# Kernel optimization log

Hardware: AMD Instinct MI355X
Metric: run time of the kernel (lower is better)

Reference implementation:

```python
import jax, jax.numpy as jnp
import numpy as np

B, T, D = 4096, 64, 256       # expressions, max tokens per expression, encoding dim
N_SYM, N_OCC = 20000, 131072  # symbols, symbol occurrences


def setup_inputs() -> dict:
    key = jax.random.key(0)
    k1, k2, k3, k4, k5 = jax.random.split(key, 5)
    # unique flattened occurrence positions -> deterministic scatter
    rng = np.random.default_rng(0)
    flat_pos = rng.permutation(B * T)[:N_OCC].astype(np.int64)
    return {
        "expressions_encodings": jax.random.normal(k1, (B, T, D), dtype=jnp.float32),
        "symbols_encodings": jax.random.normal(k2, (N_SYM, D), dtype=jnp.float32),
        "Wf": jax.random.normal(k3, (D, 2 * D), dtype=jnp.float32) * 0.05,
        "bf": jnp.zeros((D,), dtype=jnp.float32),
        "Wa": jax.random.normal(k4, (D, 2 * D), dtype=jnp.float32) * 0.05,
        "ba": jnp.zeros((D,), dtype=jnp.float32),
        "expr_idx": jnp.asarray(flat_pos // T),
        "token_idx": jnp.asarray(flat_pos % T),
        "symbol_idx": jax.random.randint(k5, (N_OCC,), 0, N_SYM, dtype=jnp.int64),
    }


def reference(expressions_encodings, symbols_encodings, Wf, bf, Wa, ba,
              expr_idx, token_idx, symbol_idx):
    b, t, d = expressions_encodings.shape
    flat = expressions_encodings.reshape(b * t, d)            # [B*T, D]
    occ_pos = t * expr_idx + token_idx                        # [N_OCC]
    prev = flat[occ_pos]                                      # gather: [N_OCC, D]
    upd = symbols_encodings[symbol_idx]                       # gather: [N_OCC, D]
    concat = jnp.concatenate([prev, upd], axis=-1)            # [N_OCC, 2D]
    forget = jax.nn.sigmoid(concat @ Wf.T + bf)               # forget gate
    add = jax.nn.sigmoid(concat @ Wa.T + ba)                  # add gate
    new_occ = forget * prev + add * upd                       # gated update
    out = flat.at[occ_pos].set(new_occ)                       # scatter back
    return out.reshape(b, t, d)
```

## Files before the change

kernel.cpp:

```cpp
#include <hip/hip_runtime.h>

typedef __attribute__((ext_vector_type(8))) short short8;
typedef __attribute__((ext_vector_type(4))) short short4v;
typedef __attribute__((ext_vector_type(4))) float floatx4;

__device__ __forceinline__ unsigned short f2bf(float f) {
    unsigned int u = __float_as_uint(f);
    u += 0x7FFFu + ((u >> 16) & 1u);
    return (unsigned short)(u >> 16);
}
__device__ __forceinline__ float bf2f(unsigned short s) {
    return __uint_as_float(((unsigned int)s) << 16);
}
__device__ __forceinline__ float sigmoidf(float x) {
    return 1.f / (1.f + __expf(-x));
}

__global__ __launch_bounds__(256)
void convert_w_kernel(const float* __restrict__ Wf,
                      const float* __restrict__ Wa,
                      short* __restrict__ wswz)
{
    int id = blockIdx.x * 256 + threadIdx.x;
    int slot = id & 63;
    int ks   = (id >> 6) & 15;
    int g    = id >> 10;
    int l15  = slot & 15, lk = slot >> 4;
    const float* base = (g < 16) ? (Wf + (long)(g * 16 + l15) * 512)
                                 : (Wa + (long)((g - 16) * 16 + l15) * 512);
    const float* src = base + ks * 32 + lk * 8;
    floatx4 w0 = *(const floatx4*)src;
    floatx4 w1 = *(const floatx4*)(src + 4);
    short8 o;
    o[0] = (short)f2bf(w0[0]); o[1] = (short)f2bf(w0[1]);
    o[2] = (short)f2bf(w0[2]); o[3] = (short)f2bf(w0[3]);
    o[4] = (short)f2bf(w1[0]); o[5] = (short)f2bf(w1[1]);
    o[6] = (short)f2bf(w1[2]); o[7] = (short)f2bf(w1[3]);
    *(short8*)(wswz + (long)id * 8) = o;
}

__global__ __launch_bounds__(256)
void mark_kernel(const int* __restrict__ ei, const int* __restrict__ ti,
                 unsigned char* __restrict__ flags, int n)
{
    int i = blockIdx.x * 256 + threadIdx.x;
    if (i < n) flags[64 * ei[i] + ti[i]] = 1;
}

__global__ __launch_bounds__(256)
void copy_rest_kernel(const float* __restrict__ flat,
                      const unsigned char* __restrict__ flags,
                      float* __restrict__ out, int nrows)
{
    const int lane = threadIdx.x & 63;
    const int w0   = (blockIdx.x * 256 + threadIdx.x) >> 6;
    const int nw   = (gridDim.x * 256) >> 6;
    for (int row = w0; row < nrows; row += nw) {
        if (flags[row]) continue;
        const floatx4* s = (const floatx4*)(flat + (long)row * 256);
        floatx4*       o = (floatx4*)(out + (long)row * 256);
        o[lane] = s[lane];
    }
}

__global__ __launch_bounds__(512, 4)
void gate_gemm_kernel(const float* __restrict__ flat,
                      const float* __restrict__ syms,
                      const float* __restrict__ bfb,
                      const float* __restrict__ bab,
                      const int* __restrict__ expr_idx,
                      const int* __restrict__ token_idx,
                      const int* __restrict__ sym_idx,
                      const short* __restrict__ wswz,
                      float* __restrict__ out)
{
    __shared__ __align__(16) short A_lds[64][520];
    __shared__ int rowbuf[64];
    __shared__ int symbuf[64];

    const int tid  = threadIdx.x;
    const int occ0 = blockIdx.x * 64;

    if (tid < 64) {
        int occ = occ0 + tid;
        rowbuf[tid] = 64 * expr_idx[occ] + token_idx[occ];
        symbuf[tid] = sym_idx[occ];
    }
    __syncthreads();

    {
        const int srow = tid >> 3;
        const int se   = tid & 7;
        const float* prow = flat + (long)rowbuf[srow] * 256;
        const float* urow = syms + (long)symbuf[srow] * 256;
        #pragma unroll
        for (int it = 0; it < 8; ++it) {
            const int k = (se + it * 8) * 4;
            floatx4 v = *(const floatx4*)(prow + k);
            short4v sv;
            sv[0] = (short)f2bf(v[0]); sv[1] = (short)f2bf(v[1]);
            sv[2] = (short)f2bf(v[2]); sv[3] = (short)f2bf(v[3]);
            *(short4v*)&A_lds[srow][k] = sv;
        }
        #pragma unroll
        for (int it = 0; it < 8; ++it) {
            const int k = (se + it * 8) * 4;
            floatx4 v = *(const floatx4*)(urow + k);
            short4v sv;
            sv[0] = (short)f2bf(v[0]); sv[1] = (short)f2bf(v[1]);
            sv[2] = (short)f2bf(v[2]); sv[3] = (short)f2bf(v[3]);
            *(short4v*)&A_lds[srow][256 + k] = sv;
        }
    }
    __syncthreads();

    const int lane = tid & 63;
    const int wv   = tid >> 6;
    const int l15  = lane & 15;
    const int lk   = lane >> 4;

    floatx4 acc[4][4];
    #pragma unroll
    for (int mi = 0; mi < 4; ++mi)
        #pragma unroll
        for (int c = 0; c < 4; ++c)
            acc[mi][c] = (floatx4){0.f, 0.f, 0.f, 0.f};

    const short8* wsv = (const short8*)wswz;

    #pragma unroll
    for (int ks = 0; ks < 16; ++ks) {
        short8 cb[4];
        #pragma unroll
        for (int mi = 0; mi < 4; ++mi)
            cb[mi] = *(const short8*)&A_lds[mi * 16 + l15][ks * 32 + lk * 8];

        #pragma unroll
        for (int c = 0; c < 4; ++c) {
            const int g = (c < 2) ? (wv * 2 + c) : (16 + wv * 2 + (c - 2));
            short8 wf = wsv[(g * 16 + ks) * 64 + lane];
            #pragma unroll
            for (int mi = 0; mi < 4; ++mi)
                acc[mi][c] = __builtin_amdgcn_mfma_f32_16x16x32_bf16(
                    wf, cb[mi], acc[mi][c], 0, 0, 0);
        }
    }

    #pragma unroll
    for (int c = 0; c < 2; ++c) {
        const int d0 = wv * 32 + c * 16 + lk * 4;
        const floatx4 bfv = *(const floatx4*)(bfb + d0);
        const floatx4 bav = *(const floatx4*)(bab + d0);
        #pragma unroll
        for (int mi = 0; mi < 4; ++mi) {
            const int m = mi * 16 + l15;
            short4v pv = *(const short4v*)&A_lds[m][d0];
            short4v uv = *(const short4v*)&A_lds[m][256 + d0];
            floatx4 res;
            #pragma unroll
            for (int j = 0; j < 4; ++j) {
                float fg = sigmoidf(acc[mi][c][j]     + bfv[j]);
                float ag = sigmoidf(acc[mi][c + 2][j] + bav[j]);
                res[j] = fg * bf2f((unsigned short)pv[j])
                       + ag * bf2f((unsigned short)uv[j]);
            }
            *(floatx4*)(out + (long)rowbuf[m] * 256 + d0) = res;
        }
    }
}

extern "C" void kernel_launch(void* const* d_in, const int* in_sizes, int n_in,
                              void* d_out, int out_size, void* d_ws, size_t ws_size,
                              hipStream_t stream) {
    const float* flat = (const float*)d_in[0];
    const float* syms = (const float*)d_in[1];
    const float* Wf   = (const float*)d_in[2];
    const float* bf   = (const float*)d_in[3];
    const float* Wa   = (const float*)d_in[4];
    const float* ba   = (const float*)d_in[5];
    const int* ei     = (const int*)d_in[6];
    const int* ti     = (const int*)d_in[7];
    const int* si     = (const int*)d_in[8];
    float* out        = (float*)d_out;

    short* wswz          = (short*)d_ws;
    unsigned char* flags = (unsigned char*)d_ws + 512 * 1024;

    const int n_occ = in_sizes[6];
    const int nrows = out_size / 256;

    hipMemsetAsync(flags, 0, nrows, stream);
    mark_kernel<<<(n_occ + 255) / 256, 256, 0, stream>>>(ei, ti, flags, n_occ);

    convert_w_kernel<<<128, 256, 0, stream>>>(Wf, Wa, wswz);

    gate_gemm_kernel<<<n_occ / 64, 512, 0, stream>>>(flat, syms, bf, ba,
                                                     ei, ti, si, wswz, out);

    copy_rest_kernel<<<2048, 256, 0, stream>>>(flat, flags, out, nrows);
}
```

Before: 241.5 us.

## Split gather into separate bf16 staging kernel and async-load it into GEMM

Splits the fused gate GEMM in two. A new gather kernel collects the prev and symbol rows, converts them to bf16, and writes a dense swizzled A matrix to workspace. The GEMM kernel then fills LDS with direct global-to-LDS async loads using an XOR swizzle to avoid bank conflicts. The aim is to take the irregular gather and conversion off the MFMA kernel's critical path, at the cost of an extra 128 MB-scale round trip through workspace plus one more launch. The old fused path stays as a fallback when the workspace is too small.

```diff
diff --git a/kernel.cpp b/kernel.cpp
--- a/kernel.cpp
+++ b/kernel.cpp
@@ -1,4 +1,5 @@
 #include <hip/hip_runtime.h>
+#include <stdint.h>
 
 typedef __attribute__((ext_vector_type(8))) short short8;
 typedef __attribute__((ext_vector_type(4))) short short4v;
@@ -14,6 +15,13 @@
 }
 __device__ __forceinline__ float sigmoidf(float x) {
     return 1.f / (1.f + __expf(-x));
+}
+
+__device__ __forceinline__ void async_load16(const short* g, short* l) {
+    __builtin_amdgcn_global_load_lds(
+        (const __attribute__((address_space(1))) unsigned int*)(uintptr_t)g,
+        (__attribute__((address_space(3))) unsigned int*)(uintptr_t)l,
+        16, 0, 0);
 }
 
 __global__ __launch_bounds__(256)
@@ -63,16 +71,132 @@
     }
 }
 
+__global__ __launch_bounds__(256)
+void gather_convert_kernel(const float* __restrict__ flat,
+                           const float* __restrict__ syms,
+                           const int* __restrict__ ei,
+                           const int* __restrict__ ti,
+                           const int* __restrict__ si,
+                           short* __restrict__ Adense, int n_occ)
+{
+    const int lane = threadIdx.x & 63;
+    const int wid  = (blockIdx.x * 256 + threadIdx.x) >> 6;
+    const int nw   = (gridDim.x * 256) >> 6;
+    for (int occ = wid; occ < n_occ; occ += nw) {
+        const int row = 64 * ei[occ] + ti[occ];
+        const int sym = si[occ];
+        const float* src = (lane < 32)
+            ? (flat + (long)row * 256 + lane * 8)
+            : (syms + (long)sym * 256 + (lane - 32) * 8);
+        floatx4 v0 = *(const floatx4*)src;
+        floatx4 v1 = *(const floatx4*)(src + 4);
+        short8 o;
+        o[0] = (short)f2bf(v0[0]); o[1] = (short)f2bf(v0[1]);
+        o[2] = (short)f2bf(v0[2]); o[3] = (short)f2bf(v0[3]);
+        o[4] = (short)f2bf(v1[0]); o[5] = (short)f2bf(v1[1]);
+        o[6] = (short)f2bf(v1[2]); o[7] = (short)f2bf(v1[3]);
+        const int co = lane ^ (occ & 7);
+        *(short8*)(Adense + (long)occ * 512 + co * 8) = o;
+    }
+}
+
 __global__ __launch_bounds__(512, 4)
-void gate_gemm_kernel(const float* __restrict__ flat,
-                      const float* __restrict__ syms,
+void gemm_gate_kernel(const short* __restrict__ Adense,
                       const float* __restrict__ bfb,
                       const float* __restrict__ bab,
                       const int* __restrict__ expr_idx,
                       const int* __restrict__ token_idx,
-                      const int* __restrict__ sym_idx,
                       const short* __restrict__ wswz,
                       float* __restrict__ out)
+{
+    __shared__ __align__(16) short A_lds[64 * 512];
+
+    const int tid  = threadIdx.x;
+    const int occ0 = blockIdx.x * 64;
+
+    {
+        const short* gbase = Adense + (long)occ0 * 512;
+        const int wub = (tid & ~63) * 8;
+        #pragma unroll
+        for (int i = 0; i < 8; ++i)
+            async_load16(gbase + i * 4096 + tid * 8, A_lds + i * 4096 + wub);
+    }
+    asm volatile("s_waitcnt vmcnt(0)" ::: "memory");
+    __syncthreads();
+
+    const int lane = tid & 63;
+    const int wv   = tid >> 6;
+    const int l15  = lane & 15;
+    const int lk   = lane >> 4;
+
+    floatx4 acc[4][4];
+    #pragma unroll
+    for (int mi = 0; mi < 4; ++mi)
+        #pragma unroll
+        for (int c = 0; c < 4; ++c)
+            acc[mi][c] = (floatx4){0.f, 0.f, 0.f, 0.f};
+
+    const short8* wsv = (const short8*)wswz;
+
+    #pragma unroll
+    for (int ks = 0; ks < 16; ++ks) {
+        short8 cb[4];
+        #pragma unroll
+        for (int mi = 0; mi < 4; ++mi) {
+            const int m = mi * 16 + l15;
+            const int ch = ((ks << 2) | lk) ^ (m & 7);
+            cb[mi] = *(const short8*)&A_lds[m * 512 + (ch << 3)];
+        }
+        #pragma unroll
+        for (int c = 0; c < 4; ++c) {
+            const int g = (c < 2) ? (wv * 2 + c) : (16 + wv * 2 + (c - 2));
+            short8 wf = wsv[(g * 16 + ks) * 64 + lane];
+            #pragma unroll
+            for (int mi = 0; mi < 4; ++mi)
+                acc[mi][c] = __builtin_amdgcn_mfma_f32_16x16x32_bf16(
+                    wf, cb[mi], acc[mi][c], 0, 0, 0);
+        }
+    }
+
+    #pragma unroll
+    for (int c = 0; c < 2; ++c) {
+        const int d0 = wv * 32 + c * 16 + lk * 4;
+        const floatx4 bfv = *(const floatx4*)(bfb + d0);
+        const floatx4 bav = *(const floatx4*)(bab + d0);
+        const int cp = d0 >> 3;
+        const int cu = 32 + (d0 >> 3);
+        const int sub = (lk & 1) * 4;
+        #pragma unroll
+        for (int mi = 0; mi < 4; ++mi) {
+            const int m = mi * 16 + l15;
+            const int sw = m & 7;
+            short4v pv = *(const short4v*)&A_lds[m * 512 + ((cp ^ sw) << 3) + sub];
+            short4v uv = *(const short4v*)&A_lds[m * 512 + ((cu ^ sw) << 3) + sub];
+            floatx4 res;
+            #pragma unroll
+            for (int j = 0; j < 4; ++j) {
+                float fg = sigmoidf(acc[mi][c][j]     + bfv[j]);
+                float ag = sigmoidf(acc[mi][c + 2][j] + bav[j]);
+                res[j] = fg * bf2f((unsigned short)pv[j])
+                       + ag * bf2f((unsigned short)uv[j]);
+            }
+            const int occ = occ0 + m;
+            const long row = 64 * expr_idx[occ] + token_idx[occ];
+            *(floatx4*)(out + row * 256 + d0) = res;
+        }
+    }
+}
+
+__global__ __launch_bounds__(512, 4)
+void gate_gemm_fused_kernel(const float* __restrict__ flat,
+                            const float* __restrict__ syms,
+                            const float* __restrict__ bfb,
+                            const float* __restrict__ bab,
+                            const int* __restrict__ expr_idx,
+                            const int* __restrict__ token_idx,
+                            const int* __restrict__ sym_idx,
+                            const short* __restrict__ wswz,
+                            float* __restrict__ out)
 {
     __shared__ __align__(16) short A_lds[64][520];
     __shared__ int rowbuf[64];
@@ -87,7 +211,6 @@
         symbuf[tid] = sym_idx[occ];
     }
     __syncthreads();
-
     {
         const int srow = tid >> 3;
         const int se   = tid & 7;
@@ -134,7 +257,6 @@
         #pragma unroll
         for (int mi = 0; mi < 4; ++mi)
             cb[mi] = *(const short8*)&A_lds[mi * 16 + l15][ks * 32 + lk * 8];
-
         #pragma unroll
         for (int c = 0; c < 4; ++c) {
             const int g = (c < 2) ? (wv * 2 + c) : (16 + wv * 2 + (c - 2));
@@ -145,7 +267,6 @@
                     wf, cb[mi], acc[mi][c], 0, 0, 0);
         }
     }
-
     #pragma unroll
     for (int c = 0; c < 2; ++c) {
         const int d0 = wv * 32 + c * 16 + lk * 4;
@@ -185,17 +306,25 @@
 
     short* wswz          = (short*)d_ws;
     unsigned char* flags = (unsigned char*)d_ws + 512 * 1024;
+    short* Adense        = (short*)((char*)d_ws + (1 << 20));
 
     const int n_occ = in_sizes[6];
     const int nrows = out_size / 256;
 
     hipMemsetAsync(flags, 0, nrows, stream);
     mark_kernel<<<(n_occ + 255) / 256, 256, 0, stream>>>(ei, ti, flags, n_occ);
-
     convert_w_kernel<<<128, 256, 0, stream>>>(Wf, Wa, wswz);
 
-    gate_gemm_kernel<<<n_occ / 64, 512, 0, stream>>>(flat, syms, bf, ba,
-                                                     ei, ti, si, wswz, out);
+    const size_t need = (size_t)(1 << 20) + (size_t)n_occ * 1024;
+    if (ws_size >= need) {
+        gather_convert_kernel<<<4096, 256, 0, stream>>>(flat, syms, ei, ti, si,
+                                                        Adense, n_occ);
+        gemm_gate_kernel<<<n_occ / 64, 512, 0, stream>>>(Adense, bf, ba,
+                                                         ei, ti, wswz, out);
+    } else {
+        gate_gemm_fused_kernel<<<n_occ / 64, 512, 0, stream>>>(
+            flat, syms, bf, ba, ei, ti, si, wswz, out);
+    }
 
     copy_rest_kernel<<<2048, 256, 0, stream>>>(flat, flags, out, nrows);
 }
```

Result: slower. 281.5 us (+16.6%).

## Make gate GEMM persistent with register-prefetched gather pipeline and swizzled LDS

Applied to the files above, without the earlier changes.

Replaces the one-tile-per-block gate GEMM with a persistent kernel of 256 blocks of 1024 threads. Each block walks several 64-occurrence tiles and prefetches the next tile's gathered rows into registers while the MFMAs for the current tile run. The A tile in LDS loses its padding and uses an XOR swizzle to avoid bank conflicts, and each wave now owns 16 output columns instead of 32. The memset is replaced with a small zeroing kernel. The trade-offs are fewer resident blocks, higher register pressure, and indices being re-read from global memory in the epilogue.

```diff
diff --git a/kernel.cpp b/kernel.cpp
--- a/kernel.cpp
+++ b/kernel.cpp
@@ -40,6 +40,12 @@
 }
 
 __global__ __launch_bounds__(256)
+void zero_flags_kernel(unsigned int* __restrict__ flags)
+{
+    flags[blockIdx.x * 256 + threadIdx.x] = 0u;
+}
+
+__global__ __launch_bounds__(256)
 void mark_kernel(const int* __restrict__ ei, const int* __restrict__ ti,
                  unsigned char* __restrict__ flags, int n)
 {
@@ -63,108 +69,131 @@
     }
 }
 
-__global__ __launch_bounds__(512, 4)
-void gate_gemm_kernel(const float* __restrict__ flat,
+__global__ __launch_bounds__(1024, 4)
+void gate_pipe_kernel(const float* __restrict__ flat,
                       const float* __restrict__ syms,
                       const float* __restrict__ bfb,
                       const float* __restrict__ bab,
-                      const int* __restrict__ expr_idx,
-                      const int* __restrict__ token_idx,
-                      const int* __restrict__ sym_idx,
+                      const int* __restrict__ ei,
+                      const int* __restrict__ ti,
+                      const int* __restrict__ si,
                       const short* __restrict__ wswz,
-                      float* __restrict__ out)
-{
-    __shared__ __align__(16) short A_lds[64][520];
-    __shared__ int rowbuf[64];
-    __shared__ int symbuf[64];
+                      float* __restrict__ out,
+                      int ntiles, int tpb)
+{
+    __shared__ __align__(16) short A_lds[64 * 512];
 
     const int tid  = threadIdx.x;
-    const int occ0 = blockIdx.x * 64;
-
-    if (tid < 64) {
-        int occ = occ0 + tid;
-        rowbuf[tid] = 64 * expr_idx[occ] + token_idx[occ];
-        symbuf[tid] = sym_idx[occ];
-    }
-    __syncthreads();
-
-    {
-        const int srow = tid >> 3;
-        const int se   = tid & 7;
-        const float* prow = flat + (long)rowbuf[srow] * 256;
-        const float* urow = syms + (long)symbuf[srow] * 256;
-        #pragma unroll
-        for (int it = 0; it < 8; ++it) {
-            const int k = (se + it * 8) * 4;
-            floatx4 v = *(const floatx4*)(prow + k);
-            short4v sv;
-            sv[0] = (short)f2bf(v[0]); sv[1] = (short)f2bf(v[1]);
-            sv[2] = (short)f2bf(v[2]); sv[3] = (short)f2bf(v[3]);
-            *(short4v*)&A_lds[srow][k] = sv;
-        }
-        #pragma unroll
-        for (int it = 0; it < 8; ++it) {
-            const int k = (se + it * 8) * 4;
-            floatx4 v = *(const floatx4*)(urow + k);
-            short4v sv;
-            sv[0] = (short)f2bf(v[0]); sv[1] = (short)f2bf(v[1]);
-            sv[2] = (short)f2bf(v[2]); sv[3] = (short)f2bf(v[3]);
-            *(short4v*)&A_lds[srow][256 + k] = sv;
-        }
-    }
-    __syncthreads();
+    const int srow = tid >> 4;
+    const int se   = tid & 15;
+    const int sw   = srow & 7;
 
     const int lane = tid & 63;
-    const int wv   = tid >> 6;
+    const int w    = tid >> 6;
     const int l15  = lane & 15;
     const int lk   = lane >> 4;
 
-    floatx4 acc[4][4];
-    #pragma unroll
-    for (int mi = 0; mi < 4; ++mi)
-        #pragma unroll
-        for (int c = 0; c < 4; ++c)
-            acc[mi][c] = (floatx4){0.f, 0.f, 0.f, 0.f};
-
+    const int tfirst = blockIdx.x * tpb;
+
+    floatx4 v[8];
+    auto issue = [&](int tile) {
+        const int occ = tile * 64 + srow;
+        const long row = 64 * ei[occ] + ti[occ];
+        const long sym = si[occ];
+        const float* pr = flat + row * 256;
+        const float* ur = syms + sym * 256;
+        v[0] = *(const floatx4*)(pr + se * 8);
+        v[1] = *(const floatx4*)(pr + se * 8 + 4);
+        v[2] = *(const floatx4*)(pr + (se + 16) * 8);
+        v[3] = *(const floatx4*)(pr + (se + 16) * 8 + 4);
+        v[4] = *(const floatx4*)(ur + se * 8);
+        v[5] = *(const floatx4*)(ur + se * 8 + 4);
+        v[6] = *(const floatx4*)(ur + (se + 16) * 8);
+        v[7] = *(const floatx4*)(ur + (se + 16) * 8 + 4);
+    };
+
+    if (tfirst < ntiles) issue(tfirst);
+
+    const int d0 = w * 16 + lk * 4;
+    const floatx4 bfv = *(const floatx4*)(bfb + d0);
+    const floatx4 bav = *(const floatx4*)(bab + d0);
     const short8* wsv = (const short8*)wswz;
 
-    #pragma unroll
-    for (int ks = 0; ks < 16; ++ks) {
-        short8 cb[4];
-        #pragma unroll
-        for (int mi = 0; mi < 4; ++mi)
-            cb[mi] = *(const short8*)&A_lds[mi * 16 + l15][ks * 32 + lk * 8];
-
-        #pragma unroll
-        for (int c = 0; c < 4; ++c) {
-            const int g = (c < 2) ? (wv * 2 + c) : (16 + wv * 2 + (c - 2));
-            short8 wf = wsv[(g * 16 + ks) * 64 + lane];
+    for (int t = 0; t < tpb; ++t) {
+        const int tile = tfirst + t;
+        if (tile >= ntiles) break;
+
+        short8 s8[4];
+        #pragma unroll
+        for (int h = 0; h < 4; ++h) {
+            floatx4 a = v[h * 2], b = v[h * 2 + 1];
+            short8 o;
+            o[0] = (short)f2bf(a[0]); o[1] = (short)f2bf(a[1]);
+            o[2] = (short)f2bf(a[2]); o[3] = (short)f2bf(a[3]);
+            o[4] = (short)f2bf(b[0]); o[5] = (short)f2bf(b[1]);
+            o[6] = (short)f2bf(b[2]); o[7] = (short)f2bf(b[3]);
+            s8[h] = o;
+        }
+
+        __syncthreads();
+
+        #pragma unroll
+        for (int h = 0; h < 4; ++h) {
+            const int chunk = (se + ((h & 1) << 4) + ((h >> 1) << 5)) ^ sw;
+            *(short8*)&A_lds[srow * 512 + chunk * 8] = s8[h];
+        }
+
+        __syncthreads();
+
+        if (t + 1 < tpb && tile + 1 < ntiles) issue(tile + 1);
+
+        floatx4 acc[4][2];
+        #pragma unroll
+        for (int mi = 0; mi < 4; ++mi) {
+            acc[mi][0] = (floatx4){0.f, 0.f, 0.f, 0.f};
+            acc[mi][1] = (floatx4){0.f, 0.f, 0.f, 0.f};
+        }
+
+        #pragma unroll
+        for (int ks = 0; ks < 16; ++ks) {
+            short8 cb[4];
+            #pragma unroll
+            for (int mi = 0; mi < 4; ++mi) {
+                const int m  = mi * 16 + l15;
+                const int ch = (ks * 4 + lk) ^ (m & 7);
+                cb[mi] = *(const short8*)&A_lds[m * 512 + ch * 8];
+            }
+            const short8 wff = wsv[(w * 16 + ks) * 64 + lane];
             #pragma unroll
             for (int mi = 0; mi < 4; ++mi)
-                acc[mi][c] = __builtin_amdgcn_mfma_f32_16x16x32_bf16(
-                    wf, cb[mi], acc[mi][c], 0, 0, 0);
-        }
-    }
-
-    #pragma unroll
-    for (int c = 0; c < 2; ++c) {
-        const int d0 = wv * 32 + c * 16 + lk * 4;
-        const floatx4 bfv = *(const floatx4*)(bfb + d0);
-        const floatx4 bav = *(const floatx4*)(bab + d0);
+                acc[mi][0] = __builtin_amdgcn_mfma_f32_16x16x32_bf16(
+                    wff, cb[mi], acc[mi][0], 0, 0, 0);
+            const short8 wfa = wsv[((16 + w) * 16 + ks) * 64 + lane];
+            #pragma unroll
+            for (int mi = 0; mi < 4; ++mi)
+                acc[mi][1] = __builtin_amdgcn_mfma_f32_16x16x32_bf16(
+                    wfa, cb[mi], acc[mi][1], 0, 0, 0);
+        }
+
         #pragma unroll
         for (int mi = 0; mi < 4; ++mi) {
-            const int m = mi * 16 + l15;
-            short4v pv = *(const short4v*)&A_lds[m][d0];
-            short4v uv = *(const short4v*)&A_lds[m][256 + d0];
+            const int m   = mi * 16 + l15;
+            const int occ = tile * 64 + m;
+            const long row = 64 * ei[occ] + ti[occ];
+            const int cp = (d0 >> 3) ^ (m & 7);
+            const int cu = (32 + (d0 >> 3)) ^ (m & 7);
+            const int sub = d0 & 7;
+            short4v pv = *(const short4v*)&A_lds[m * 512 + cp * 8 + sub];
+            short4v uv = *(const short4v*)&A_lds[m * 512 + cu * 8 + sub];
             floatx4 res;
             #pragma unroll
             for (int j = 0; j < 4; ++j) {
-                float fg = sigmoidf(acc[mi][c][j]     + bfv[j]);
-                float ag = sigmoidf(acc[mi][c + 2][j] + bav[j]);
+                float fg = sigmoidf(acc[mi][0][j] + bfv[j]);
+                float ag = sigmoidf(acc[mi][1][j] + bav[j]);
                 res[j] = fg * bf2f((unsigned short)pv[j])
                        + ag * bf2f((unsigned short)uv[j]);
             }
-            *(floatx4*)(out + (long)rowbuf[m] * 256 + d0) = res;
+            *(floatx4*)(out + row * 256 + d0) = res;
         }
     }
 }
@@ -189,13 +218,16 @@
     const int n_occ = in_sizes[6];
     const int nrows = out_size / 256;
 
-    hipMemsetAsync(flags, 0, nrows, stream);
+    zero_flags_kernel<<<nrows / 1024, 256, 0, stream>>>((unsigned int*)flags);
     mark_kernel<<<(n_occ + 255) / 256, 256, 0, stream>>>(ei, ti, flags, n_occ);
-
     convert_w_kernel<<<128, 256, 0, stream>>>(Wf, Wa, wswz);
 
-    gate_gemm_kernel<<<n_occ / 64, 512, 0, stream>>>(flat, syms, bf, ba,
-                                                     ei, ti, si, wswz, out);
+    const int ntiles = n_occ / 64;
+    const int nblk   = 256;
+    const int tpb    = (ntiles + nblk - 1) / nblk;
+    gate_pipe_kernel<<<nblk, 1024, 0, stream>>>(flat, syms, bf, ba,
+                                                ei, ti, si, wswz, out,
+                                                ntiles, tpb);
 
     copy_rest_kernel<<<2048, 256, 0, stream>>>(flat, flags, out, nrows);
 }
```

Result: slower. 304.5 us (+26.1%).

## Fuse copy-rest into gate GEMM kernel with interleaved blocks and swizzled LDS

Applied to the files above, without the earlier changes.

Merges the untouched-row copy kernel into the gate GEMM launch, interleaving copy blocks among GEMM tiles so the copy traffic overlaps with compute and one launch is saved. The A tile is stored densely in LDS with an XOR swizzle in place of padding. Weight fragments are prefetched one k-step ahead, and the M dimension is processed in two halves to cut accumulator registers. The memset is replaced by a small zeroing kernel. Costs are extra index reloads in the epilogue and a more complex block-role mapping.

```diff
diff --git a/kernel.cpp b/kernel.cpp
--- a/kernel.cpp
+++ b/kernel.cpp
@@ -40,6 +40,12 @@
 }
 
 __global__ __launch_bounds__(256)
+void zero_flags_kernel(unsigned int* __restrict__ flags)
+{
+    flags[blockIdx.x * 256 + threadIdx.x] = 0u;
+}
+
+__global__ __launch_bounds__(256)
 void mark_kernel(const int* __restrict__ ei, const int* __restrict__ ti,
                  unsigned char* __restrict__ flags, int n)
 {
@@ -47,124 +53,155 @@
     if (i < n) flags[64 * ei[i] + ti[i]] = 1;
 }
 
-__global__ __launch_bounds__(256)
-void copy_rest_kernel(const float* __restrict__ flat,
-                      const unsigned char* __restrict__ flags,
-                      float* __restrict__ out, int nrows)
-{
-    const int lane = threadIdx.x & 63;
-    const int w0   = (blockIdx.x * 256 + threadIdx.x) >> 6;
-    const int nw   = (gridDim.x * 256) >> 6;
-    for (int row = w0; row < nrows; row += nw) {
-        if (flags[row]) continue;
-        const floatx4* s = (const floatx4*)(flat + (long)row * 256);
-        floatx4*       o = (floatx4*)(out + (long)row * 256);
-        o[lane] = s[lane];
-    }
-}
-
 __global__ __launch_bounds__(512, 4)
-void gate_gemm_kernel(const float* __restrict__ flat,
-                      const float* __restrict__ syms,
-                      const float* __restrict__ bfb,
-                      const float* __restrict__ bab,
-                      const int* __restrict__ expr_idx,
-                      const int* __restrict__ token_idx,
-                      const int* __restrict__ sym_idx,
-                      const short* __restrict__ wswz,
-                      float* __restrict__ out)
-{
-    __shared__ __align__(16) short A_lds[64][520];
-    __shared__ int rowbuf[64];
-    __shared__ int symbuf[64];
-
-    const int tid  = threadIdx.x;
-    const int occ0 = blockIdx.x * 64;
-
-    if (tid < 64) {
-        int occ = occ0 + tid;
-        rowbuf[tid] = 64 * expr_idx[occ] + token_idx[occ];
-        symbuf[tid] = sym_idx[occ];
+void main_kernel(const float* __restrict__ flat,
+                 const float* __restrict__ syms,
+                 const float* __restrict__ bfb,
+                 const float* __restrict__ bab,
+                 const int* __restrict__ ei,
+                 const int* __restrict__ ti,
+                 const int* __restrict__ si,
+                 const short* __restrict__ wswz,
+                 const unsigned char* __restrict__ flags,
+                 float* __restrict__ out,
+                 int ntiles, int ncopy)
+{
+    __shared__ __align__(16) short A_lds[64 * 512];
+
+    const int bid   = blockIdx.x;
+    const int total = ntiles + ncopy;
+    const int tid   = threadIdx.x;
+    const int lane  = tid & 63;
+    const int w     = tid >> 6;
+
+    const int c_before = (int)(((long)bid * ncopy) / total);
+    const bool is_copy = (int)(((long)(bid + 1) * ncopy) / total) > c_before;
+
+    if (is_copy) {
+        const int r0 = c_before * 256;
+        for (int it = 0; it < 32; ++it) {
+            const int row = r0 + it * 8 + w;
+            if (flags[row]) continue;
+            const floatx4* s = (const floatx4*)(flat + (long)row * 256);
+            floatx4*       o = (floatx4*)(out + (long)row * 256);
+            o[lane] = s[lane];
+        }
+        return;
+    }
+
+    const int tile = bid - c_before;
+    const int occ0 = tile * 64;
+
+    {
+        int rowi[8], symi[8];
+        #pragma unroll
+        for (int i = 0; i < 8; ++i) {
+            const int occ = occ0 + w * 8 + i;
+            rowi[i] = 64 * ei[occ] + ti[occ];
+            symi[i] = si[occ];
+        }
+        floatx4 va[8], vb[8];
+        #pragma unroll
+        for (int i = 0; i < 8; ++i) {
+            const float* base = (lane < 32)
+                ? (flat + (long)rowi[i] * 256 + lane * 8)
+                : (syms + (long)symi[i] * 256 + (lane - 32) * 8);
+            va[i] = *(const floatx4*)base;
+            vb[i] = *(const floatx4*)(base + 4);
+        }
+        #pragma unroll
+        for (int i = 0; i < 8; ++i) {
+            short8 o;
+            o[0] = (short)f2bf(va[i][0]); o[1] = (short)f2bf(va[i][1]);
+            o[2] = (short)f2bf(va[i][2]); o[3] = (short)f2bf(va[i][3]);
+            o[4] = (short)f2bf(vb[i][0]); o[5] = (short)f2bf(vb[i][1]);
+            o[6] = (short)f2bf(vb[i][2]); o[7] = (short)f2bf(vb[i][3]);
+            const int r = w * 8 + i;
+            *(short8*)&A_lds[r * 512 + ((lane ^ (r & 7)) << 3)] = o;
+        }
     }
     __syncthreads();
 
-    {
-        const int srow = tid >> 3;
-        const int se   = tid & 7;
-        const float* prow = flat + (long)rowbuf[srow] * 256;
-        const float* urow = syms + (long)symbuf[srow] * 256;
-        #pragma unroll
-        for (int it = 0; it < 8; ++it) {
-            const int k = (se + it * 8) * 4;
-            floatx4 v = *(const floatx4*)(prow + k);
-            short4v sv;
-            sv[0] = (short)f2bf(v[0]); sv[1] = (short)f2bf(v[1]);
-            sv[2] = (short)f2bf(v[2]); sv[3] = (short)f2bf(v[3]);
-            *(short4v*)&A_lds[srow][k] = sv;
-        }
-        #pragma unroll
-        for (int it = 0; it < 8; ++it) {
-            const int k = (se + it * 8) * 4;
-            floatx4 v = *(const floatx4*)(urow + k);
-            short4v sv;
-            sv[0] = (short)f2bf(v[0]); sv[1] = (short)f2bf(v[1]);
-            sv[2] = (short)f2bf(v[2]); sv[3] = (short)f2bf(v[3]);
-            *(short4v*)&A_lds[srow][256 + k] = sv;
-        }
-    }
-    __syncthreads();
-
-    const int lane = tid & 63;
-    const int wv   = tid >> 6;
-    const int l15  = lane & 15;
-    const int lk   = lane >> 4;
-
-    floatx4 acc[4][4];
-    #pragma unroll
-    for (int mi = 0; mi < 4; ++mi)
-        #pragma unroll
-        for (int c = 0; c < 4; ++c)
-            acc[mi][c] = (floatx4){0.f, 0.f, 0.f, 0.f};
-
+    const int l15 = lane & 15;
+    const int lk  = lane >> 4;
     const short8* wsv = (const short8*)wswz;
 
-    #pragma unroll
-    for (int ks = 0; ks < 16; ++ks) {
-        short8 cb[4];
-        #pragma unroll
-        for (int mi = 0; mi < 4; ++mi)
-            cb[mi] = *(const short8*)&A_lds[mi * 16 + l15][ks * 32 + lk * 8];
-
-        #pragma unroll
-        for (int c = 0; c < 4; ++c) {
-            const int g = (c < 2) ? (wv * 2 + c) : (16 + wv * 2 + (c - 2));
-            short8 wf = wsv[(g * 16 + ks) * 64 + lane];
-            #pragma unroll
-            for (int mi = 0; mi < 4; ++mi)
-                acc[mi][c] = __builtin_amdgcn_mfma_f32_16x16x32_bf16(
-                    wf, cb[mi], acc[mi][c], 0, 0, 0);
-        }
-    }
-
+    floatx4 bfv[2], bav[2];
     #pragma unroll
     for (int c = 0; c < 2; ++c) {
-        const int d0 = wv * 32 + c * 16 + lk * 4;
-        const floatx4 bfv = *(const floatx4*)(bfb + d0);
-        const floatx4 bav = *(const floatx4*)(bab + d0);
-        #pragma unroll
-        for (int mi = 0; mi < 4; ++mi) {
-            const int m = mi * 16 + l15;
-            short4v pv = *(const short4v*)&A_lds[m][d0];
-            short4v uv = *(const short4v*)&A_lds[m][256 + d0];
-            floatx4 res;
-            #pragma unroll
-            for (int j = 0; j < 4; ++j) {
-                float fg = sigmoidf(acc[mi][c][j]     + bfv[j]);
-                float ag = sigmoidf(acc[mi][c + 2][j] + bav[j]);
-                res[j] = fg * bf2f((unsigned short)pv[j])
-                       + ag * bf2f((unsigned short)uv[j]);
-            }
-            *(floatx4*)(out + (long)rowbuf[m] * 256 + d0) = res;
+        const int d0 = w * 32 + c * 16 + lk * 4;
+        bfv[c] = *(const floatx4*)(bfb + d0);
+        bav[c] = *(const floatx4*)(bab + d0);
+    }
+
+    #pragma unroll
+    for (int h = 0; h < 2; ++h) {
+        floatx4 acc[2][4];
+        #pragma unroll
+        for (int mi = 0; mi < 2; ++mi)
+            #pragma unroll
+            for (int c = 0; c < 4; ++c)
+                acc[mi][c] = (floatx4){0.f, 0.f, 0.f, 0.f};
+
+        short8 wfc[4];
+        #pragma unroll
+        for (int c = 0; c < 4; ++c) {
+            const int g = (c < 2) ? (w * 2 + c) : (16 + w * 2 + (c - 2));
+            wfc[c] = wsv[(g * 16 + 0) * 64 + lane];
+        }
+
+        #pragma unroll
+        for (int ks = 0; ks < 16; ++ks) {
+            short8 cb[2];
+            #pragma unroll
+            for (int mi = 0; mi < 2; ++mi) {
+                const int m  = (h * 2 + mi) * 16 + l15;
+                const int ch = (ks * 4 + lk) ^ (m & 7);
+                cb[mi] = *(const short8*)&A_lds[m * 512 + (ch << 3)];
+            }
+            short8 wfn[4];
+            if (ks < 15) {
+                #pragma unroll
+                for (int c = 0; c < 4; ++c) {
+                    const int g = (c < 2) ? (w * 2 + c) : (16 + w * 2 + (c - 2));
+                    wfn[c] = wsv[(g * 16 + ks + 1) * 64 + lane];
+                }
+            }
+            #pragma unroll
+            for (int c = 0; c < 4; ++c)
+                #pragma unroll
+                for (int mi = 0; mi < 2; ++mi)
+                    acc[mi][c] = __builtin_amdgcn_mfma_f32_16x16x32_bf16(
+                        wfc[c], cb[mi], acc[mi][c], 0, 0, 0);
+            if (ks < 15) {
+                #pragma unroll
+                for (int c = 0; c < 4; ++c) wfc[c] = wfn[c];
+            }
+        }
+
+        #pragma unroll
+        for (int mi = 0; mi < 2; ++mi) {
+            const int m   = (h * 2 + mi) * 16 + l15;
+            const int occ = occ0 + m;
+            const long row = 64 * ei[occ] + ti[occ];
+            const int sw  = m & 7;
+            #pragma unroll
+            for (int c = 0; c < 2; ++c) {
+                const int d0 = w * 32 + c * 16 + lk * 4;
+                const int cp = (d0 >> 3) ^ sw;
+                const int cu = (32 + (d0 >> 3)) ^ sw;
+                short4v pv = *(const short4v*)&A_lds[m * 512 + (cp << 3) + (d0 & 7)];
+                short4v uv = *(const short4v*)&A_lds[m * 512 + (cu << 3) + (d0 & 7)];
+                floatx4 res;
+                #pragma unroll
+                for (int j = 0; j < 4; ++j) {
+                    float fg = sigmoidf(acc[mi][c][j]     + bfv[c][j]);
+                    float ag = sigmoidf(acc[mi][c + 2][j] + bav[c][j]);
+                    res[j] = fg * bf2f((unsigned short)pv[j])
+                           + ag * bf2f((unsigned short)uv[j]);
+                }
+                *(floatx4*)(out + row * 256 + d0) = res;
+            }
         }
     }
 }
@@ -189,13 +226,13 @@
     const int n_occ = in_sizes[6];
     const int nrows = out_size / 256;
 
-    hipMemsetAsync(flags, 0, nrows, stream);
+    zero_flags_kernel<<<nrows / 1024, 256, 0, stream>>>((unsigned int*)flags);
     mark_kernel<<<(n_occ + 255) / 256, 256, 0, stream>>>(ei, ti, flags, n_occ);
-
     convert_w_kernel<<<128, 256, 0, stream>>>(Wf, Wa, wswz);
 
-    gate_gemm_kernel<<<n_occ / 64, 512, 0, stream>>>(flat, syms, bf, ba,
-                                                     ei, ti, si, wswz, out);
-
-    copy_rest_kernel<<<2048, 256, 0, stream>>>(flat, flags, out, nrows);
-}
+    const int ntiles = n_occ / 64;
+    const int ncopy  = nrows / 256;
+    main_kernel<<<ntiles + ncopy, 512, 0, stream>>>(flat, syms, bf, ba,
+                                                    ei, ti, si, wswz, flags,
+                                                    out, ntiles, ncopy);
+}
```

Result: slower. 297.8 us (+23.3%).
